# Kernel tuning notes

Measured on AMD Instinct MI355X. Metric: run time of the kernel, lower is better.

The kernel has to match this reference:

```python
import jax, jax.numpy as jnp
import numpy as np

N = 100000   # nodes
E = 1600000  # edges
F_IN = 64    # input features
H = 64       # hidden channels
C = 40       # classes


def setup_inputs() -> dict:
    key = jax.random.key(0)
    k1, k2, k3, k4 = jax.random.split(key, 4)
    x = jax.random.normal(k1, (N, F_IN), dtype=jnp.float32)
    edge_index = jax.random.randint(k2, (2, E), 0, N, dtype=jnp.int64)
    W1 = jax.random.normal(k3, (F_IN, H), dtype=jnp.float32) / np.sqrt(F_IN)
    b1 = jnp.zeros((H,), dtype=jnp.float32)
    W2 = jax.random.normal(k4, (H, C), dtype=jnp.float32) / np.sqrt(H)
    b2 = jnp.zeros((C,), dtype=jnp.float32)
    return {"x": x, "edge_index": edge_index, "W1": W1, "b1": b1, "W2": W2, "b2": b2}


def gcn_conv(x, src, dst, W, b):
    """PyG-style GCNConv: self-loops + symmetric deg^{-1/2} normalization.
    src/dst already include self-loops. x: [N, Fin], W: [Fin, Fout]."""
    n = x.shape[0]
    deg = jax.ops.segment_sum(jnp.ones_like(dst, dtype=x.dtype), dst, num_segments=n)
    dinv = jnp.where(deg > 0, jax.lax.rsqrt(deg), jnp.zeros_like(deg))
    norm = dinv[src] * dinv[dst]          # [E+N]
    h = x @ W                             # transform first (Fin -> Fout)
    msg = h[src] * norm[:, None]          # gather + scale, [E+N, Fout]
    out = jax.ops.segment_sum(msg, dst, num_segments=n)  # scatter-add
    return out + b


def reference(x, edge_index, W1, b1, W2, b2):
    n = x.shape[0]
    loops = jnp.arange(n, dtype=edge_index.dtype)
    src = jnp.concatenate([edge_index[0], loops])
    dst = jnp.concatenate([edge_index[1], loops])
    h = jax.nn.relu(gcn_conv(x, src, dst, W1, b1))
    # F.dropout in eval mode (training=False) is identity
    out = gcn_conv(h, src, dst, W2, b2)
    return jax.nn.log_softmax(out, axis=1)
```

## Files before the change

kernel.cpp:

```cpp
#include <hip/hip_runtime.h>
#include <math.h>

#define F1 64
#define F2 40
#define NB 1024
#define TILE 4096
#define FCAP 3200

typedef unsigned int uint;
typedef __attribute__((ext_vector_type(8))) short s8v;
typedef __attribute__((ext_vector_type(4))) float f4v;

union U8 { s8v s; uint4 q; uint u[4]; };

__device__ inline unsigned short f2bf(float f) {
    unsigned u = __float_as_uint(f);
    unsigned r = (u + 0x7FFFu + ((u >> 16) & 1u)) >> 16;
    return (unsigned short)r;
}
__device__ inline uint packbf(float lo, float hi) {
    return (uint)f2bf(lo) | ((uint)f2bf(hi) << 16);
}
__device__ inline float bf_lo(uint u) { return __uint_as_float(u << 16); }
__device__ inline float bf_hi(uint u) { return __uint_as_float(u & 0xFFFF0000u); }

__device__ inline void split2(float a, float b, uint* hu, uint* lu) {
    unsigned short ha = f2bf(a), hb = f2bf(b);
    *hu = (uint)ha | ((uint)hb << 16);
    float ra = a - __uint_as_float((uint)ha << 16);
    float rb = b - __uint_as_float((uint)hb << 16);
    *lu = packbf(ra, rb);
}

__global__ __launch_bounds__(256) void k_bhist(const int* __restrict__ dst,
                                               int* __restrict__ bcnt, int e, int bsh) {
    __shared__ int h[NB];
    int tid = threadIdx.x;
    for (int i = tid; i < NB; i += 256) h[i] = 0;
    __syncthreads();
    int base = blockIdx.x * TILE;
    int lim = min(base + TILE, e);
    for (int i = base + tid; i < lim; i += 256) atomicAdd(&h[dst[i] >> bsh], 1);
    __syncthreads();
    for (int i = tid; i < NB; i += 256) if (h[i]) atomicAdd(&bcnt[i], h[i]);
}

__global__ __launch_bounds__(NB) void k_bscan(const int* __restrict__ bcnt,
                                              int* __restrict__ bptr, int* __restrict__ gcur,
                                              int* __restrict__ row_ptr, int n, int e) {
    __shared__ int sh[NB];
    int t = threadIdx.x;
    sh[t] = bcnt[t];
    __syncthreads();
    for (int off = 1; off < NB; off <<= 1) {
        int v = (t >= off) ? sh[t - off] : 0;
        __syncthreads();
        sh[t] += v;
        __syncthreads();
    }
    int ex = t ? sh[t - 1] : 0;
    bptr[t] = ex;
    gcur[t] = ex;
    if (t == NB - 1) bptr[NB] = sh[NB - 1];
    if (t == 0) row_ptr[n] = e;
}

__global__ __launch_bounds__(256) void k_bscatter(const int* __restrict__ src,
                                                  const int* __restrict__ dst,
                                                  int* gcur,
                                                  unsigned long long* __restrict__ pairs,
                                                  int e, int bsh) {
    __shared__ int lhist[NB];
    __shared__ int lstart[NB];
    __shared__ int delta[NB];
    __shared__ unsigned long long stage[TILE];
    int tid = threadIdx.x;
    for (int i = tid; i < NB; i += 256) lhist[i] = 0;
    __syncthreads();
    int base = blockIdx.x * TILE;
    int cnt = min(TILE, e - base);
    int sA[16], dA[16], rA[16];
#pragma unroll
    for (int k = 0; k < 16; ++k) {
        int i = base + k * 256 + tid;
        if (i < e) {
            sA[k] = src[i];
            dA[k] = dst[i];
            rA[k] = atomicAdd(&lhist[dA[k] >> bsh], 1);
        }
    }
    __syncthreads();
    if (tid < 64) {
        const int per = NB / 64;
        int v[per];
        int b0 = tid * per, s = 0;
#pragma unroll
        for (int j = 0; j < per; ++j) { v[j] = lhist[b0 + j]; s += v[j]; }
        int sc = s;
        for (int o = 1; o < 64; o <<= 1) { int u = __shfl_up(sc, o); if (tid >= o) sc += u; }
        int ex = sc - s;
#pragma unroll
        for (int j = 0; j < per; ++j) { lstart[b0 + j] = ex; ex += v[j]; }
    }
    __syncthreads();
    for (int i = tid; i < NB; i += 256) {
        int c = lhist[i];
        if (c) delta[i] = atomicAdd(&gcur[i], c) - lstart[i];
    }
    __syncthreads();
#pragma unroll
    for (int k = 0; k < 16; ++k) {
        int i = base + k * 256 + tid;
        if (i < e) {
            int b = dA[k] >> bsh;
            stage[lstart[b] + rA[k]] =
                ((unsigned long long)(unsigned)sA[k] << 32) | (unsigned)dA[k];
        }
    }
    __syncthreads();
    for (int p = tid; p < cnt; p += 256) {
        unsigned long long pr = stage[p];
        int b = ((int)(unsigned)pr) >> bsh;
        pairs[delta[b] + p] = pr;
    }
}

__global__ __launch_bounds__(256) void k_final(const unsigned long long* __restrict__ pairs,
                                               const int* __restrict__ bptr,
                                               int* __restrict__ srcs,
                                               int* __restrict__ row_ptr,
                                               float* __restrict__ dinv,
                                               int n, int bsh) {
    __shared__ int ldeg[128];
    __shared__ int lrow[128];
    __shared__ int lcur[128];
    __shared__ unsigned long long stg[FCAP];
    int b = blockIdx.x, tid = threadIdx.x;
    int beg = bptr[b], cnt = bptr[b + 1] - beg;
    int node0 = b << bsh;
    int bnodes = 1 << bsh;
    for (int i = tid; i < bnodes; i += 256) { ldeg[i] = 0; lcur[i] = 0; }
    bool fit = cnt <= FCAP;
    __syncthreads();
    if (fit) {
        for (int p = tid; p < cnt; p += 256) {
            unsigned long long pr = pairs[beg + p];
            stg[p] = pr;
            atomicAdd(&ldeg[((int)(unsigned)pr) - node0], 1);
        }
    } else {
        for (int p = tid; p < cnt; p += 256)
            atomicAdd(&ldeg[((int)(unsigned)pairs[beg + p]) - node0], 1);
    }
    __syncthreads();
    if (tid < 64) {
        int per = bnodes >> 6;
        int b0 = tid * per, s = 0;
        for (int j = 0; j < per; ++j) s += ldeg[b0 + j];
        int sc = s;
        for (int o = 1; o < 64; o <<= 1) { int u = __shfl_up(sc, o); if (tid >= o) sc += u; }
        int ex = sc - s;
        for (int j = 0; j < per; ++j) { lrow[b0 + j] = ex; ex += ldeg[b0 + j]; }
    }
    __syncthreads();
    for (int i = tid; i < bnodes; i += 256) {
        int node = node0 + i;
        if (node < n) {
            row_ptr[node] = beg + lrow[i];
            dinv[node] = rsqrtf((float)(ldeg[i] + 1));
        }
    }
    if (fit) {
        for (int p = tid; p < cnt; p += 256) {
            unsigned long long pr = stg[p];
            int dl = ((int)(unsigned)pr) - node0;
            int r = atomicAdd(&lcur[dl], 1);
            srcs[beg + lrow[dl] + r] = (int)(pr >> 32);
        }
    } else {
        for (int p = tid; p < cnt; p += 256) {
            unsigned long long pr = pairs[beg + p];
            int dl = ((int)(unsigned)pr) - node0;
            int r = atomicAdd(&lcur[dl], 1);
            srcs[beg + lrow[dl] + r] = (int)(pr >> 32);
        }
    }
}

__global__ __launch_bounds__(256) void k_wprep(const float* __restrict__ W1,
                                               const float* __restrict__ W2,
                                               uint4* __restrict__ wf1,
                                               uint4* __restrict__ wf2) {
    int g = blockIdx.x * 256 + threadIdx.x;
    if (g < 512) {
        int ks = g >> 8, ct = (g >> 6) & 3, l = g & 63;
        int c = 16 * ct + (l & 15);
        int kb = 32 * ks + 8 * (l >> 4);
        uint hu[4], lu[4];
#pragma unroll
        for (int i = 0; i < 4; ++i)
            split2(W1[(kb + 2 * i) * 64 + c], W1[(kb + 2 * i + 1) * 64 + c], &hu[i], &lu[i]);
        wf1[(size_t)(ks * 4 + ct) * 64 + l]       = make_uint4(hu[0], hu[1], hu[2], hu[3]);
        wf1[(size_t)((2 + ks) * 4 + ct) * 64 + l] = make_uint4(lu[0], lu[1], lu[2], lu[3]);
    } else if (g < 896) {
        int v = g - 512;
        int ks = v / 192, rem = v % 192;
        int ct = rem >> 6, l = rem & 63;
        int c = 16 * ct + (l & 15);
        int kb = 32 * ks + 8 * (l >> 4);
        uint hu[4], lu[4];
#pragma unroll
        for (int i = 0; i < 4; ++i) {
            float a = (c < 40) ? W2[(kb + 2 * i) * 40 + c] : 0.0f;
            float b = (c < 40) ? W2[(kb + 2 * i + 1) * 40 + c] : 0.0f;
            split2(a, b, &hu[i], &lu[i]);
        }
        wf2[(size_t)(ks * 3 + ct) * 64 + l]       = make_uint4(hu[0], hu[1], hu[2], hu[3]);
        wf2[(size_t)((2 + ks) * 3 + ct) * 64 + l] = make_uint4(lu[0], lu[1], lu[2], lu[3]);
    }
}

__global__ __launch_bounds__(256) void k_gemm1(const float* __restrict__ x,
                                               const uint4* __restrict__ wf1,
                                               const float* __restrict__ dinv,
                                               unsigned short* __restrict__ h, int n) {
    int w = threadIdx.x >> 6, l = threadIdx.x & 63;
    int node0 = blockIdx.x * 64 + w * 16;
    int ar = min(node0 + (l & 15), n - 1);
    const float* ap = x + (size_t)ar * 64 + 8 * (l >> 4);
    float4 a0 = *(const float4*)ap;
    float4 a1 = *(const float4*)(ap + 4);
    float4 a2 = *(const float4*)(ap + 32);
    float4 a3 = *(const float4*)(ap + 36);
    U8 ah0, al0, ah1, al1;
    split2(a0.x, a0.y, &ah0.u[0], &al0.u[0]);
    split2(a0.z, a0.w, &ah0.u[1], &al0.u[1]);
    split2(a1.x, a1.y, &ah0.u[2], &al0.u[2]);
    split2(a1.z, a1.w, &ah0.u[3], &al0.u[3]);
    split2(a2.x, a2.y, &ah1.u[0], &al1.u[0]);
    split2(a2.z, a2.w, &ah1.u[1], &al1.u[1]);
    split2(a3.x, a3.y, &ah1.u[2], &al1.u[2]);
    split2(a3.z, a3.w, &ah1.u[3], &al1.u[3]);
    f4v acc[4];
#pragma unroll
    for (int ct = 0; ct < 4; ++ct) acc[ct] = (f4v){0.0f, 0.0f, 0.0f, 0.0f};
#pragma unroll
    for (int ct = 0; ct < 4; ++ct) {
        U8 bh0, bh1, bl0, bl1;
        bh0.q = wf1[(size_t)(0 * 4 + ct) * 64 + l];
        bh1.q = wf1[(size_t)(1 * 4 + ct) * 64 + l];
        bl0.q = wf1[(size_t)(2 * 4 + ct) * 64 + l];
        bl1.q = wf1[(size_t)(3 * 4 + ct) * 64 + l];
        acc[ct] = __builtin_amdgcn_mfma_f32_16x16x32_bf16(ah0.s, bh0.s, acc[ct], 0, 0, 0);
        acc[ct] = __builtin_amdgcn_mfma_f32_16x16x32_bf16(ah1.s, bh1.s, acc[ct], 0, 0, 0);
        acc[ct] = __builtin_amdgcn_mfma_f32_16x16x32_bf16(al0.s, bh0.s, acc[ct], 0, 0, 0);
        acc[ct] = __builtin_amdgcn_mfma_f32_16x16x32_bf16(al1.s, bh1.s, acc[ct], 0, 0, 0);
        acc[ct] = __builtin_amdgcn_mfma_f32_16x16x32_bf16(ah0.s, bl0.s, acc[ct], 0, 0, 0);
        acc[ct] = __builtin_amdgcn_mfma_f32_16x16x32_bf16(ah1.s, bl1.s, acc[ct], 0, 0, 0);
    }
    int r0 = node0 + (l >> 4) * 4;
    float dv[4];
#pragma unroll
    for (int r = 0; r < 4; ++r) dv[r] = dinv[min(r0 + r, n - 1)];
#pragma unroll
    for (int ct = 0; ct < 4; ++ct)
#pragma unroll
        for (int r = 0; r < 4; ++r)
            if (r0 + r < n)
                h[(size_t)(r0 + r) * 64 + 16 * ct + (l & 15)] = f2bf(acc[ct][r] * dv[r]);
}

__global__ __launch_bounds__(256) void k_gat(const uint4* __restrict__ h4,
                                             const int* __restrict__ srcs,
                                             const int* __restrict__ row_ptr,
                                             const float* __restrict__ dinv,
                                             const float* __restrict__ b,
                                             const uint4* __restrict__ wf2,
                                             unsigned short* __restrict__ t, int n) {
    __shared__ uint agg[64][36];
    int tid = threadIdx.x;
    int lane = tid & 63;
    int l32 = lane & 31;
    int hw = lane & 32;
    int slot = l32 >> 3, j = l32 & 7;
    int nbase = blockIdx.x * 64;
#pragma unroll 1
    for (int rnd = 0; rnd < 8; ++rnd) {
        int nl = rnd * 8 + (tid >> 5);
        int node = nbase + nl;
        if (node < n) {
            int e0 = row_ptr[node], cnt = row_ptr[node + 1] - e0;
            int idx = (l32 < cnt) ? srcs[e0 + l32] : 0;
            float a0x=0,a0y=0,a1x=0,a1y=0,a2x=0,a2y=0,a3x=0,a3y=0;
            if (slot == 0) {
                uint4 u = h4[(size_t)node * 8 + j];
                a0x = bf_lo(u.x); a0y = bf_hi(u.x);
                a1x = bf_lo(u.y); a1y = bf_hi(u.y);
                a2x = bf_lo(u.z); a2y = bf_hi(u.z);
                a3x = bf_lo(u.w); a3y = bf_hi(u.w);
            }
            int cl = max(min(cnt, 32) - 1, 0);
#pragma unroll
            for (int i = 0; i < 8; ++i) {
                int e = slot + 4 * i;
                int sv = __shfl(idx, hw + min(e, cl));
                uint4 u = h4[(size_t)sv * 8 + j];
                if (e < cnt) {
                    a0x += bf_lo(u.x);  a0y += bf_hi(u.x);
                    a1x += bf_lo(u.y);  a1y += bf_hi(u.y);
                    a2x += bf_lo(u.z);  a2y += bf_hi(u.z);
                    a3x += bf_lo(u.w);  a3y += bf_hi(u.w);
                }
            }
            for (int p = 32 + slot; p < cnt; p += 4) {
                int s0 = srcs[e0 + p];
                uint4 u0 = h4[(size_t)s0 * 8 + j];
                a0x += bf_lo(u0.x);  a0y += bf_hi(u0.x);
                a1x += bf_lo(u0.y);  a1y += bf_hi(u0.y);
                a2x += bf_lo(u0.z);  a2y += bf_hi(u0.z);
                a3x += bf_lo(u0.w);  a3y += bf_hi(u0.w);
            }
#define COMB(o) \
            a0x += __shfl_xor(a0x, o); a0y += __shfl_xor(a0y, o); \
            a1x += __shfl_xor(a1x, o); a1y += __shfl_xor(a1y, o); \
            a2x += __shfl_xor(a2x, o); a2y += __shfl_xor(a2y, o); \
            a3x += __shfl_xor(a3x, o); a3y += __shfl_xor(a3y, o);
            COMB(8) COMB(16)
#undef COMB
            if (slot == 0) {
                float di = dinv[node];
                float4 bl = *(const float4*)&b[8 * j];
                float4 bh = *(const float4*)&b[8 * j + 4];
                float v0 = fmaxf(fmaf(a0x, di, bl.x), 0.0f);
                float v1 = fmaxf(fmaf(a0y, di, bl.y), 0.0f);
                float v2 = fmaxf(fmaf(a1x, di, bl.z), 0.0f);
                float v3 = fmaxf(fmaf(a1y, di, bl.w), 0.0f);
                float v4 = fmaxf(fmaf(a2x, di, bh.x), 0.0f);
                float v5 = fmaxf(fmaf(a2y, di, bh.y), 0.0f);
                float v6 = fmaxf(fmaf(a3x, di, bh.z), 0.0f);
                float v7 = fmaxf(fmaf(a3y, di, bh.w), 0.0f);
                uint4 r;
                r.x = packbf(v0, v1); r.y = packbf(v2, v3);
                r.z = packbf(v4, v5); r.w = packbf(v6, v7);
                *(uint4*)&agg[nl][4 * j] = r;
            }
        }
    }
    __syncthreads();
    int w = tid >> 6, l = tid & 63;
    int node0 = nbase + w * 16;
    int nl = w * 16 + (l & 15);
    U8 a0, a1;
    a0.q = *(const uint4*)&agg[nl][4 * (l >> 4)];
    a1.q = *(const uint4*)&agg[nl][16 + 4 * (l >> 4)];
    f4v acc[3];
#pragma unroll
    for (int ct = 0; ct < 3; ++ct) acc[ct] = (f4v){0.0f, 0.0f, 0.0f, 0.0f};
#pragma unroll
    for (int ct = 0; ct < 3; ++ct) {
        U8 bh0, bh1, bl0, bl1;
        bh0.q = wf2[(size_t)(0 * 3 + ct) * 64 + l];
        bh1.q = wf2[(size_t)(1 * 3 + ct) * 64 + l];
        bl0.q = wf2[(size_t)(2 * 3 + ct) * 64 + l];
        bl1.q = wf2[(size_t)(3 * 3 + ct) * 64 + l];
        acc[ct] = __builtin_amdgcn_mfma_f32_16x16x32_bf16(a0.s, bh0.s, acc[ct], 0, 0, 0);
        acc[ct] = __builtin_amdgcn_mfma_f32_16x16x32_bf16(a1.s, bh1.s, acc[ct], 0, 0, 0);
        acc[ct] = __builtin_amdgcn_mfma_f32_16x16x32_bf16(a0.s, bl0.s, acc[ct], 0, 0, 0);
        acc[ct] = __builtin_amdgcn_mfma_f32_16x16x32_bf16(a1.s, bl1.s, acc[ct], 0, 0, 0);
    }
    int r0 = node0 + (l >> 4) * 4;
    float dv[4];
#pragma unroll
    for (int r = 0; r < 4; ++r) dv[r] = dinv[min(r0 + r, n - 1)];
#pragma unroll
    for (int ct = 0; ct < 3; ++ct) {
        int col = 16 * ct + (l & 15);
#pragma unroll
        for (int r = 0; r < 4; ++r)
            if (col < 40 && r0 + r < n)
                t[(size_t)(r0 + r) * 40 + col] = f2bf(acc[ct][r] * dv[r]);
    }
}

__global__ __launch_bounds__(256) void k_gather40(const uint2* __restrict__ t2,
                                                  const int* __restrict__ srcs,
                                                  const int* __restrict__ row_ptr,
                                                  const float* __restrict__ dinv,
                                                  const float* __restrict__ b2,
                                                  float* __restrict__ out, int n) {
    int node = (int)(((long long)blockIdx.x * 256 + threadIdx.x) >> 5);
    int lane = threadIdx.x & 63;
    int l32 = lane & 31;
    int hw = lane & 32;
    if (node >= n) return;
    int slot = l32 / 10;
    int j = l32 - slot * 10;
    int e0 = row_ptr[node];
    int cnt = row_ptr[node + 1] - e0;
    int idx = (l32 < cnt && l32 < 30) ? srcs[e0 + l32] : 0;
    float a0=0, a1=0, a2=0, a3=0;
    if (slot == 0) {
        uint2 u = t2[(size_t)node * 10 + j];
        a0 = bf_lo(u.x); a1 = bf_hi(u.x);
        a2 = bf_lo(u.y); a3 = bf_hi(u.y);
    }
    if (slot < 3) {
        int cl = max(min(cnt, 30) - 1, 0);
#pragma unroll
        for (int i = 0; i < 10; ++i) {
            int e = slot + 3 * i;
            int sv = __shfl(idx, hw + min(e, cl));
            uint2 u = t2[(size_t)sv * 10 + j];
            if (e < cnt) {
                a0 += bf_lo(u.x);  a1 += bf_hi(u.x);
                a2 += bf_lo(u.y);  a3 += bf_hi(u.y);
            }
        }
        for (int p = 30 + slot; p < cnt; p += 3) {
            int s0 = srcs[e0 + p];
            uint2 u0 = t2[(size_t)s0 * 10 + j];
            a0 += bf_lo(u0.x);  a1 += bf_hi(u0.x);
            a2 += bf_lo(u0.y);  a3 += bf_hi(u0.y);
        }
    }
    float t0 = a0 + __shfl(a0, lane + 10) + __shfl(a0, lane + 20);
    float t1 = a1 + __shfl(a1, lane + 10) + __shfl(a1, lane + 20);
    float t2s = a2 + __shfl(a2, lane + 10) + __shfl(a2, lane + 20);
    float t3 = a3 + __shfl(a3, lane + 10) + __shfl(a3, lane + 20);
    bool actc = l32 < 10;
    float di = dinv[node];
    float4 bb = actc ? *(const float4*)&b2[4 * l32] : make_float4(0, 0, 0, 0);
    float v0 = fmaf(t0, di, bb.x);
    float v1 = fmaf(t1, di, bb.y);
    float v2 = fmaf(t2s, di, bb.z);
    float v3 = fmaf(t3, di, bb.w);
    float mv = actc ? fmaxf(fmaxf(v0, v1), fmaxf(v2, v3)) : -INFINITY;
    for (int o = 16; o; o >>= 1) mv = fmaxf(mv, __shfl_xor(mv, o));
    float ex = actc ? (expf(v0 - mv) + expf(v1 - mv) + expf(v2 - mv) + expf(v3 - mv)) : 0.0f;
    float s = ex;
    for (int o = 16; o; o >>= 1) s += __shfl_xor(s, o);
    float ls = mv + logf(s);
    if (actc) {
        float4 r = make_float4(v0 - ls, v1 - ls, v2 - ls, v3 - ls);
        *(float4*)&out[(size_t)node * 40 + 4 * l32] = r;
    }
}

extern "C" void kernel_launch(void* const* d_in, const int* in_sizes, int n_in,
                              void* d_out, int out_size, void* d_ws, size_t ws_size,
                              hipStream_t stream) {
    const float* x  = (const float*)d_in[0];
    const int*   ei = (const int*)d_in[1];
    const float* W1 = (const float*)d_in[2];
    const float* b1 = (const float*)d_in[3];
    const float* W2 = (const float*)d_in[4];
    const float* b2 = (const float*)d_in[5];

    const int N = in_sizes[0] / F1;
    const int E = in_sizes[1] / 2;
    const int* src = ei;
    const int* dst = ei + E;

    int bsh = 7;
    while ((((N - 1) >> bsh) + 1) > NB) ++bsh;
    const int NBu = ((N - 1) >> bsh) + 1;

    uint4* h1b     = (uint4*)d_ws;
    uint2* tb      = (uint2*)(h1b + (size_t)N * 8);
    uint4* wf1     = (uint4*)(tb + (size_t)N * 10);
    uint4* wf2     = wf1 + 1024;
    unsigned long long* pairs = (unsigned long long*)(wf2 + 768);
    int*   srcs    = (int*)(pairs + E);
    int*   row_ptr = srcs + E;
    float* dinv    = (float*)(row_ptr + N + 1);
    int*   bcnt    = (int*)(dinv + N);
    int*   bptr    = bcnt + NB;
    int*   gcur    = bptr + NB + 1;
    float* outp    = (float*)d_out;

    const int B = 256;
    const int GT = (E + TILE - 1) / TILE;

    k_wprep<<<4, B, 0, stream>>>(W1, W2, wf1, wf2);

    hipMemsetAsync(bcnt, 0, NB * sizeof(int), stream);
    k_bhist<<<GT, B, 0, stream>>>(dst, bcnt, E, bsh);
    k_bscan<<<1, NB, 0, stream>>>(bcnt, bptr, gcur, row_ptr, N, E);
    k_bscatter<<<GT, B, 0, stream>>>(src, dst, gcur, pairs, E, bsh);
    k_final<<<NBu, B, 0, stream>>>(pairs, bptr, srcs, row_ptr, dinv, N, bsh);

    const int GM = (N + 63) / 64;

    k_gemm1<<<GM, B, 0, stream>>>(x, wf1, dinv, (unsigned short*)h1b, N);
    k_gat<<<GM, B, 0, stream>>>(h1b, srcs, row_ptr, dinv, b1, wf2,
                                (unsigned short*)tb, N);

    k_gather40<<<(N + 7) / 8, B, 0, stream>>>(tb, srcs, row_ptr, dinv, b2, outp, N);
}
```

Before: 234.2 us.

## Fuse layer-1 GEMM into bucket scatter kernel and pack edge pairs to 32 bits

Makes the first-layer GEMM independent of dinv by applying the source-side normalization inside the aggregation kernel. The GEMM blocks can then run in the same launch as the bucket scatter, which removes one launch and lets the GEMM overlap the sort. Edge pairs are also packed into 32-bit words (source shifted left by bsh, OR'd with the destination's offset inside its bucket), which halves pair traffic and the shared staging in k_final. The cost is an extra dinv gather per edge in the aggregation, plus heavier shared-memory use in the fused kernel, since GEMM blocks also reserve the scatter's LDS and this may limit occupancy.

```diff
diff --git a/kernel.cpp b/kernel.cpp
--- a/kernel.cpp
+++ b/kernel.cpp
@@ -65,67 +65,115 @@
     if (t == 0) row_ptr[n] = e;
 }
 
-__global__ __launch_bounds__(256) void k_bscatter(const int* __restrict__ src,
-                                                  const int* __restrict__ dst,
-                                                  int* gcur,
-                                                  unsigned long long* __restrict__ pairs,
-                                                  int e, int bsh) {
+__global__ __launch_bounds__(256) void k_bsg(const int* __restrict__ src,
+                                             const int* __restrict__ dst,
+                                             int* gcur, uint* __restrict__ pairs,
+                                             int e, int bsh, int gt,
+                                             const float* __restrict__ x,
+                                             const uint4* __restrict__ wf1,
+                                             unsigned short* __restrict__ h, int n) {
     __shared__ int lhist[NB];
     __shared__ int lstart[NB];
     __shared__ int delta[NB];
     __shared__ unsigned long long stage[TILE];
     int tid = threadIdx.x;
-    for (int i = tid; i < NB; i += 256) lhist[i] = 0;
-    __syncthreads();
-    int base = blockIdx.x * TILE;
-    int cnt = min(TILE, e - base);
-    int sA[16], dA[16], rA[16];
-#pragma unroll
-    for (int k = 0; k < 16; ++k) {
-        int i = base + k * 256 + tid;
-        if (i < e) {
-            sA[k] = src[i];
-            dA[k] = dst[i];
-            rA[k] = atomicAdd(&lhist[dA[k] >> bsh], 1);
-        }
-    }
-    __syncthreads();
-    if (tid < 64) {
-        const int per = NB / 64;
-        int v[per];
-        int b0 = tid * per, s = 0;
-#pragma unroll
-        for (int j = 0; j < per; ++j) { v[j] = lhist[b0 + j]; s += v[j]; }
-        int sc = s;
-        for (int o = 1; o < 64; o <<= 1) { int u = __shfl_up(sc, o); if (tid >= o) sc += u; }
-        int ex = sc - s;
-#pragma unroll
-        for (int j = 0; j < per; ++j) { lstart[b0 + j] = ex; ex += v[j]; }
-    }
-    __syncthreads();
-    for (int i = tid; i < NB; i += 256) {
-        int c = lhist[i];
-        if (c) delta[i] = atomicAdd(&gcur[i], c) - lstart[i];
-    }
-    __syncthreads();
-#pragma unroll
-    for (int k = 0; k < 16; ++k) {
-        int i = base + k * 256 + tid;
-        if (i < e) {
-            int b = dA[k] >> bsh;
-            stage[lstart[b] + rA[k]] =
-                ((unsigned long long)(unsigned)sA[k] << 32) | (unsigned)dA[k];
-        }
-    }
-    __syncthreads();
-    for (int p = tid; p < cnt; p += 256) {
-        unsigned long long pr = stage[p];
-        int b = ((int)(unsigned)pr) >> bsh;
-        pairs[delta[b] + p] = pr;
-    }
-}
-
-__global__ __launch_bounds__(256) void k_final(const unsigned long long* __restrict__ pairs,
+    if (blockIdx.x < gt) {
+        int msk = (1 << bsh) - 1;
+        for (int i = tid; i < NB; i += 256) lhist[i] = 0;
+        __syncthreads();
+        int base = blockIdx.x * TILE;
+        int cnt = min(TILE, e - base);
+        int sA[16], dA[16], rA[16];
+#pragma unroll
+        for (int k = 0; k < 16; ++k) {
+            int i = base + k * 256 + tid;
+            if (i < e) {
+                sA[k] = src[i];
+                dA[k] = dst[i];
+                rA[k] = atomicAdd(&lhist[dA[k] >> bsh], 1);
+            }
+        }
+        __syncthreads();
+        if (tid < 64) {
+            const int per = NB / 64;
+            int v[per];
+            int b0 = tid * per, s = 0;
+#pragma unroll
+            for (int j = 0; j < per; ++j) { v[j] = lhist[b0 + j]; s += v[j]; }
+            int sc = s;
+            for (int o = 1; o < 64; o <<= 1) { int u = __shfl_up(sc, o); if (tid >= o) sc += u; }
+            int ex = sc - s;
+#pragma unroll
+            for (int j = 0; j < per; ++j) { lstart[b0 + j] = ex; ex += v[j]; }
+        }
+        __syncthreads();
+        for (int i = tid; i < NB; i += 256) {
+            int c = lhist[i];
+            if (c) delta[i] = atomicAdd(&gcur[i], c) - lstart[i];
+        }
+        __syncthreads();
+#pragma unroll
+        for (int k = 0; k < 16; ++k) {
+            int i = base + k * 256 + tid;
+            if (i < e) {
+                int b = dA[k] >> bsh;
+                stage[lstart[b] + rA[k]] =
+                    ((unsigned long long)(unsigned)sA[k] << 32) | (unsigned)dA[k];
+            }
+        }
+        __syncthreads();
+        for (int p = tid; p < cnt; p += 256) {
+            unsigned long long pr = stage[p];
+            int d = (int)(unsigned)pr;
+            int b = d >> bsh;
+            pairs[delta[b] + p] = ((uint)(pr >> 32) << bsh) | (uint)(d & msk);
+        }
+    } else {
+        int w = tid >> 6, l = tid & 63;
+        int node0 = (blockIdx.x - gt) * 64 + w * 16;
+        int ar = min(node0 + (l & 15), n - 1);
+        const float* ap = x + (size_t)ar * 64 + 8 * (l >> 4);
+        float4 a0 = *(const float4*)ap;
+        float4 a1 = *(const float4*)(ap + 4);
+        float4 a2 = *(const float4*)(ap + 32);
+        float4 a3 = *(const float4*)(ap + 36);
+        U8 ah0, al0, ah1, al1;
+        split2(a0.x, a0.y, &ah0.u[0], &al0.u[0]);
+        split2(a0.z, a0.w, &ah0.u[1], &al0.u[1]);
+        split2(a1.x, a1.y, &ah0.u[2], &al0.u[2]);
+        split2(a1.z, a1.w, &ah0.u[3], &al0.u[3]);
+        split2(a2.x, a2.y, &ah1.u[0], &al1.u[0]);
+        split2(a2.z, a2.w, &ah1.u[1], &al1.u[1]);
+        split2(a3.x, a3.y, &ah1.u[2], &al1.u[2]);
+        split2(a3.z, a3.w, &ah1.u[3], &al1.u[3]);
+        f4v acc[4];
+#pragma unroll
+        for (int ct = 0; ct < 4; ++ct) acc[ct] = (f4v){0.0f, 0.0f, 0.0f, 0.0f};
+#pragma unroll
+        for (int ct = 0; ct < 4; ++ct) {
+            U8 bh0, bh1, bl0, bl1;
+            bh0.q = wf1[(size_t)(0 * 4 + ct) * 64 + l];
+            bh1.q = wf1[(size_t)(1 * 4 + ct) * 64 + l];
+            bl0.q = wf1[(size_t)(2 * 4 + ct) * 64 + l];
+            bl1.q = wf1[(size_t)(3 * 4 + ct) * 64 + l];
+            acc[ct] = __builtin_amdgcn_mfma_f32_16x16x32_bf16(ah0.s, bh0.s, acc[ct], 0, 0, 0);
+            acc[ct] = __builtin_amdgcn_mfma_f32_16x16x32_bf16(ah1.s, bh1.s, acc[ct], 0, 0, 0);
+            acc[ct] = __builtin_amdgcn_mfma_f32_16x16x32_bf16(al0.s, bh0.s, acc[ct], 0, 0, 0);
+            acc[ct] = __builtin_amdgcn_mfma_f32_16x16x32_bf16(al1.s, bh1.s, acc[ct], 0, 0, 0);
+            acc[ct] = __builtin_amdgcn_mfma_f32_16x16x32_bf16(ah0.s, bl0.s, acc[ct], 0, 0, 0);
+            acc[ct] = __builtin_amdgcn_mfma_f32_16x16x32_bf16(ah1.s, bl1.s, acc[ct], 0, 0, 0);
+        }
+        int r0 = node0 + (l >> 4) * 4;
+#pragma unroll
+        for (int ct = 0; ct < 4; ++ct)
+#pragma unroll
+            for (int r = 0; r < 4; ++r)
+                if (r0 + r < n)
+                    h[(size_t)(r0 + r) * 64 + 16 * ct + (l & 15)] = f2bf(acc[ct][r]);
+    }
+}
+
+__global__ __launch_bounds__(256) void k_final(const uint* __restrict__ pairs,
                                                const int* __restrict__ bptr,
                                                int* __restrict__ srcs,
                                                int* __restrict__ row_ptr,
@@ -134,23 +182,24 @@
     __shared__ int ldeg[128];
     __shared__ int lrow[128];
     __shared__ int lcur[128];
-    __shared__ unsigned long long stg[FCAP];
+    __shared__ uint stg[FCAP];
     int b = blockIdx.x, tid = threadIdx.x;
     int beg = bptr[b], cnt = bptr[b + 1] - beg;
     int node0 = b << bsh;
     int bnodes = 1 << bsh;
+    int msk = bnodes - 1;
     for (int i = tid; i < bnodes; i += 256) { ldeg[i] = 0; lcur[i] = 0; }
     bool fit = cnt <= FCAP;
     __syncthreads();
     if (fit) {
         for (int p = tid; p < cnt; p += 256) {
-            unsigned long long pr = pairs[beg + p];
+            uint pr = pairs[beg + p];
             stg[p] = pr;
-            atomicAdd(&ldeg[((int)(unsigned)pr) - node0], 1);
+            atomicAdd(&ldeg[pr & msk], 1);
         }
     } else {
         for (int p = tid; p < cnt; p += 256)
-            atomicAdd(&ldeg[((int)(unsigned)pairs[beg + p]) - node0], 1);
+            atomicAdd(&ldeg[pairs[beg + p] & msk], 1);
     }
     __syncthreads();
     if (tid < 64) {
@@ -172,17 +221,17 @@
     }
     if (fit) {
         for (int p = tid; p < cnt; p += 256) {
-            unsigned long long pr = stg[p];
-            int dl = ((int)(unsigned)pr) - node0;
+            uint pr = stg[p];
+            int dl = pr & msk;
             int r = atomicAdd(&lcur[dl], 1);
-            srcs[beg + lrow[dl] + r] = (int)(pr >> 32);
+            srcs[beg + lrow[dl] + r] = (int)(pr >> bsh);
         }
     } else {
         for (int p = tid; p < cnt; p += 256) {
-            unsigned long long pr = pairs[beg + p];
-            int dl = ((int)(unsigned)pr) - node0;
+            uint pr = pairs[beg + p];
+            int dl = pr & msk;
             int r = atomicAdd(&lcur[dl], 1);
-            srcs[beg + lrow[dl] + r] = (int)(pr >> 32);
+            srcs[beg + lrow[dl] + r] = (int)(pr >> bsh);
         }
     }
 }
@@ -218,56 +267,6 @@
         wf2[(size_t)(ks * 3 + ct) * 64 + l]       = make_uint4(hu[0], hu[1], hu[2], hu[3]);
         wf2[(size_t)((2 + ks) * 3 + ct) * 64 + l] = make_uint4(lu[0], lu[1], lu[2], lu[3]);
     }
-}
-
-__global__ __launch_bounds__(256) void k_gemm1(const float* __restrict__ x,
-                                               const uint4* __restrict__ wf1,
-                                               const float* __restrict__ dinv,
-                                               unsigned short* __restrict__ h, int n) {
-    int w = threadIdx.x >> 6, l = threadIdx.x & 63;
-    int node0 = blockIdx.x * 64 + w * 16;
-    int ar = min(node0 + (l & 15), n - 1);
-    const float* ap = x + (size_t)ar * 64 + 8 * (l >> 4);
-    float4 a0 = *(const float4*)ap;
-    float4 a1 = *(const float4*)(ap + 4);
-    float4 a2 = *(const float4*)(ap + 32);
-    float4 a3 = *(const float4*)(ap + 36);
-    U8 ah0, al0, ah1, al1;
-    split2(a0.x, a0.y, &ah0.u[0], &al0.u[0]);
-    split2(a0.z, a0.w, &ah0.u[1], &al0.u[1]);
-    split2(a1.x, a1.y, &ah0.u[2], &al0.u[2]);
-    split2(a1.z, a1.w, &ah0.u[3], &al0.u[3]);
-    split2(a2.x, a2.y, &ah1.u[0], &al1.u[0]);
-    split2(a2.z, a2.w, &ah1.u[1], &al1.u[1]);
-    split2(a3.x, a3.y, &ah1.u[2], &al1.u[2]);
-    split2(a3.z, a3.w, &ah1.u[3], &al1.u[3]);
-    f4v acc[4];
-#pragma unroll
-    for (int ct = 0; ct < 4; ++ct) acc[ct] = (f4v){0.0f, 0.0f, 0.0f, 0.0f};
-#pragma unroll
-    for (int ct = 0; ct < 4; ++ct) {
-        U8 bh0, bh1, bl0, bl1;
-        bh0.q = wf1[(size_t)(0 * 4 + ct) * 64 + l];
-        bh1.q = wf1[(size_t)(1 * 4 + ct) * 64 + l];
-        bl0.q = wf1[(size_t)(2 * 4 + ct) * 64 + l];
-        bl1.q = wf1[(size_t)(3 * 4 + ct) * 64 + l];
-        acc[ct] = __builtin_amdgcn_mfma_f32_16x16x32_bf16(ah0.s, bh0.s, acc[ct], 0, 0, 0);
-        acc[ct] = __builtin_amdgcn_mfma_f32_16x16x32_bf16(ah1.s, bh1.s, acc[ct], 0, 0, 0);
-        acc[ct] = __builtin_amdgcn_mfma_f32_16x16x32_bf16(al0.s, bh0.s, acc[ct], 0, 0, 0);
-        acc[ct] = __builtin_amdgcn_mfma_f32_16x16x32_bf16(al1.s, bh1.s, acc[ct], 0, 0, 0);
-        acc[ct] = __builtin_amdgcn_mfma_f32_16x16x32_bf16(ah0.s, bl0.s, acc[ct], 0, 0, 0);
-        acc[ct] = __builtin_amdgcn_mfma_f32_16x16x32_bf16(ah1.s, bl1.s, acc[ct], 0, 0, 0);
-    }
-    int r0 = node0 + (l >> 4) * 4;
-    float dv[4];
-#pragma unroll
-    for (int r = 0; r < 4; ++r) dv[r] = dinv[min(r0 + r, n - 1)];
-#pragma unroll
-    for (int ct = 0; ct < 4; ++ct)
-#pragma unroll
-        for (int r = 0; r < 4; ++r)
-            if (r0 + r < n)
-                h[(size_t)(r0 + r) * 64 + 16 * ct + (l & 15)] = f2bf(acc[ct][r] * dv[r]);
 }
 
 __global__ __launch_bounds__(256) void k_gat(const uint4* __restrict__ h4,
@@ -291,34 +290,39 @@
         if (node < n) {
             int e0 = row_ptr[node], cnt = row_ptr[node + 1] - e0;
             int idx = (l32 < cnt) ? srcs[e0 + l32] : 0;
+            float dvp = dinv[idx];
+            float di = dinv[node];
             float a0x=0,a0y=0,a1x=0,a1y=0,a2x=0,a2y=0,a3x=0,a3y=0;
             if (slot == 0) {
                 uint4 u = h4[(size_t)node * 8 + j];
-                a0x = bf_lo(u.x); a0y = bf_hi(u.x);
-                a1x = bf_lo(u.y); a1y = bf_hi(u.y);
-                a2x = bf_lo(u.z); a2y = bf_hi(u.z);
-                a3x = bf_lo(u.w); a3y = bf_hi(u.w);
+                a0x = bf_lo(u.x) * di; a0y = bf_hi(u.x) * di;
+                a1x = bf_lo(u.y) * di; a1y = bf_hi(u.y) * di;
+                a2x = bf_lo(u.z) * di; a2y = bf_hi(u.z) * di;
+                a3x = bf_lo(u.w) * di; a3y = bf_hi(u.w) * di;
             }
             int cl = max(min(cnt, 32) - 1, 0);
 #pragma unroll
             for (int i = 0; i < 8; ++i) {
                 int e = slot + 4 * i;
-                int sv = __shfl(idx, hw + min(e, cl));
+                int q = hw + min(e, cl);
+                int sv = __shfl(idx, q);
+                float ds = __shfl(dvp, q);
                 uint4 u = h4[(size_t)sv * 8 + j];
                 if (e < cnt) {
-                    a0x += bf_lo(u.x);  a0y += bf_hi(u.x);
-                    a1x += bf_lo(u.y);  a1y += bf_hi(u.y);
-                    a2x += bf_lo(u.z);  a2y += bf_hi(u.z);
-                    a3x += bf_lo(u.w);  a3y += bf_hi(u.w);
+                    a0x = fmaf(bf_lo(u.x), ds, a0x);  a0y = fmaf(bf_hi(u.x), ds, a0y);
+                    a1x = fmaf(bf_lo(u.y), ds, a1x);  a1y = fmaf(bf_hi(u.y), ds, a1y);
+                    a2x = fmaf(bf_lo(u.z), ds, a2x);  a2y = fmaf(bf_hi(u.z), ds, a2y);
+                    a3x = fmaf(bf_lo(u.w), ds, a3x);  a3y = fmaf(bf_hi(u.w), ds, a3y);
                 }
             }
             for (int p = 32 + slot; p < cnt; p += 4) {
                 int s0 = srcs[e0 + p];
+                float ds = dinv[s0];
                 uint4 u0 = h4[(size_t)s0 * 8 + j];
-                a0x += bf_lo(u0.x);  a0y += bf_hi(u0.x);
-                a1x += bf_lo(u0.y);  a1y += bf_hi(u0.y);
-                a2x += bf_lo(u0.z);  a2y += bf_hi(u0.z);
-                a3x += bf_lo(u0.w);  a3y += bf_hi(u0.w);
+                a0x = fmaf(bf_lo(u0.x), ds, a0x);  a0y = fmaf(bf_hi(u0.x), ds, a0y);
+                a1x = fmaf(bf_lo(u0.y), ds, a1x);  a1y = fmaf(bf_hi(u0.y), ds, a1y);
+                a2x = fmaf(bf_lo(u0.z), ds, a2x);  a2y = fmaf(bf_hi(u0.z), ds, a2y);
+                a3x = fmaf(bf_lo(u0.w), ds, a3x);  a3y = fmaf(bf_hi(u0.w), ds, a3y);
             }
 #define COMB(o) \
             a0x += __shfl_xor(a0x, o); a0y += __shfl_xor(a0y, o); \
@@ -328,7 +332,6 @@
             COMB(8) COMB(16)
 #undef COMB
             if (slot == 0) {
-                float di = dinv[node];
                 float4 bl = *(const float4*)&b[8 * j];
                 float4 bh = *(const float4*)&b[8 * j + 4];
                 float v0 = fmaxf(fmaf(a0x, di, bl.x), 0.0f);
@@ -469,7 +472,7 @@
     uint2* tb      = (uint2*)(h1b + (size_t)N * 8);
     uint4* wf1     = (uint4*)(tb + (size_t)N * 10);
     uint4* wf2     = wf1 + 1024;
-    unsigned long long* pairs = (unsigned long long*)(wf2 + 768);
+    uint*  pairs   = (uint*)(wf2 + 768);
     int*   srcs    = (int*)(pairs + E);
     int*   row_ptr = srcs + E;
     float* dinv    = (float*)(row_ptr + N + 1);
@@ -480,18 +483,17 @@
 
     const int B = 256;
     const int GT = (E + TILE - 1) / TILE;
+    const int GM = (N + 63) / 64;
 
     k_wprep<<<4, B, 0, stream>>>(W1, W2, wf1, wf2);
 
     hipMemsetAsync(bcnt, 0, NB * sizeof(int), stream);
     k_bhist<<<GT, B, 0, stream>>>(dst, bcnt, E, bsh);
     k_bscan<<<1, NB, 0, stream>>>(bcnt, bptr, gcur, row_ptr, N, E);
-    k_bscatter<<<GT, B, 0, stream>>>(src, dst, gcur, pairs, E, bsh);
+    k_bsg<<<GT + GM, B, 0, stream>>>(src, dst, gcur, pairs, E, bsh, GT,
+                                     x, wf1, (unsigned short*)h1b, N);
     k_final<<<NBu, B, 0, stream>>>(pairs, bptr, srcs, row_ptr, dinv, N, bsh);
 
-    const int GM = (N + 63) / 64;
-
-    k_gemm1<<<GM, B, 0, stream>>>(x, wf1, dinv, (unsigned short*)h1b, N);
     k_gat<<<GM, B, 0, stream>>>(h1b, srcs, row_ptr, dinv, b1, wf2,
                                 (unsigned short*)tb, N);
 
```

After: 228.4 us, median of 2. 1.03x faster.
